# Performance work log

Measured on AMD Instinct MI355X. Metric: run time of the kernel, lower is better.

## Reference

```python
import jax, jax.numpy as jnp
import numpy as np

Q_DIM, T_DIM, TOP_M, TEMP = 512, 768, 5, 0.07
B, H, W, K = 8, 64, 64, 128
LN_EPS = 1e-5

def _layernorm(x, g, b):
    mu = jnp.mean(x, axis=-1, keepdims=True)
    var = jnp.mean(jnp.square(x - mu), axis=-1, keepdims=True)
    return (x - mu) * jax.lax.rsqrt(var + LN_EPS) * g + b

def _l2norm(x):
    n = jnp.linalg.norm(x, axis=-1, keepdims=True)
    return x / jnp.maximum(n, 1e-12)

def setup_inputs() -> dict:
    key = jax.random.key(0)
    ks = jax.random.split(key, 12)
    s = lambda d: 1.0 / np.sqrt(d)
    return {
        'visual_features': jax.random.normal(ks[0], (B, H, W, Q_DIM), jnp.float32),
        'text_features': jax.random.normal(ks[1], (B, K, T_DIM), jnp.float32),
        'Wq': jax.random.uniform(ks[2], (Q_DIM, T_DIM), jnp.float32, -s(Q_DIM), s(Q_DIM)),
        'bq': jnp.zeros((T_DIM,), jnp.float32),
        'Wv': jax.random.uniform(ks[3], (T_DIM, Q_DIM), jnp.float32, -s(T_DIM), s(T_DIM)),
        'bv': jnp.zeros((Q_DIM,), jnp.float32),
        'W1': jax.random.uniform(ks[4], (Q_DIM, 4 * Q_DIM), jnp.float32, -s(Q_DIM), s(Q_DIM)),
        'b1': jnp.zeros((4 * Q_DIM,), jnp.float32),
        'W2': jax.random.uniform(ks[5], (4 * Q_DIM, Q_DIM), jnp.float32, -s(4 * Q_DIM), s(4 * Q_DIM)),
        'b2': jnp.zeros((Q_DIM,), jnp.float32),
        'g1': jnp.ones((Q_DIM,), jnp.float32), 'be1': jnp.zeros((Q_DIM,), jnp.float32),
        'g2': jnp.ones((Q_DIM,), jnp.float32), 'be2': jnp.zeros((Q_DIM,), jnp.float32),
    }

def reference(visual_features, text_features, Wq, bq, Wv, bv, W1, b1, W2, b2, g1, be1, g2, be2):
    b, h, w, c = visual_features.shape
    residual = visual_features.reshape(b, h * w, c)
    vis = _layernorm(residual, g1, be1)                      # (B,N,C)
    query = _l2norm(vis @ Wq + bq)                            # (B,N,Ct)
    keyt = _l2norm(text_features)                             # (B,K,Ct)
    value = text_features @ Wv + bv                           # (B,K,C)
    sim = jnp.einsum('bnc,bkc->bnk', query, keyt)             # (B,N,K)
    # top-M sparsification: keep top_m logits, others -> -inf
    top_v = jax.lax.top_k(sim, TOP_M)[0]                      # (B,N,M) sorted desc
    thr = top_v[..., -1:]
    sim = jnp.where(sim >= thr, sim, -jnp.inf)
    attn = jax.nn.softmax(sim / TEMP, axis=-1)
    aligned = jnp.einsum('bnk,bkc->bnc', attn, value)
    fused = residual + aligned
    fused = _layernorm(fused, g2, be2)
    ffn = jax.nn.gelu(fused @ W1 + b1, approximate=False) @ W2 + b2
    out = fused + ffn
    return out.reshape(b, h, w, c)
```

## Files before the change

kernel.cpp:

```cpp
#include <hip/hip_runtime.h>
#include <math.h>

typedef unsigned short u16;
typedef unsigned int   u32;
typedef unsigned long long u64;
typedef __attribute__((ext_vector_type(4))) float f32x4;
typedef __attribute__((ext_vector_type(4))) unsigned int u32x4;
typedef __attribute__((ext_vector_type(8))) _Float16 f16x8;
typedef __attribute__((ext_vector_type(8))) short s16x8;

#define NROWS   32768
#define CDIM    512
#define TDIM    768
#define KKEY    128
#define FFDIM   2048
#define NB      8
#define RPB     4096
#define LN_EPS_ 1e-5f
#define TINV    (1.0f/0.07f)
#define RESCUE_MARGIN 1e-5f

__device__ __forceinline__ u16 f2h(float f){ _Float16 h=(_Float16)f; return __builtin_bit_cast(u16,h); }
__device__ __forceinline__ float h2f(u16 v){ return (float)__builtin_bit_cast(_Float16, v); }
__device__ __forceinline__ unsigned pk2(float a,float b){ return (unsigned)f2h(a)|((unsigned)f2h(b)<<16); }
__device__ __forceinline__ u16 f2b(float f){
  u32 u = __builtin_bit_cast(u32, f);
  u32 r = (u + 0x7fffu + ((u>>16)&1u)) >> 16;
  return (u16)r;
}
__device__ __forceinline__ float b2f(u16 h){ u32 u = ((u32)h)<<16; return __builtin_bit_cast(float, u); }
__device__ __forceinline__ unsigned pkb(float a,float b){ return (unsigned)f2b(a)|((unsigned)f2b(b)<<16); }

__device__ __forceinline__ void gl_lds16(const void* g, void* l){
  __builtin_amdgcn_global_load_lds(
      (const __attribute__((address_space(1))) u32*)g,
      (__attribute__((address_space(3))) u32*)l, 16, 0, 0);
}

__device__ __forceinline__ float fast_exp2(float x){
#if __has_builtin(__builtin_amdgcn_exp2f)
  return __builtin_amdgcn_exp2f(x);
#else
  return exp2f(x);
#endif
}
__device__ __forceinline__ float fast_rcp(float x){
#if __has_builtin(__builtin_amdgcn_rcpf)
  return __builtin_amdgcn_rcpf(x);
#else
  return 1.0f/x;
#endif
}

__device__ __forceinline__ float wsumf(float v){
#pragma unroll
  for(int o=1;o<64;o<<=1) v+=__shfl_xor(v,o);
  return v; }
__device__ __forceinline__ float wmaxf(float v){
#pragma unroll
  for(int o=1;o<64;o<<=1) v=fmaxf(v,__shfl_xor(v,o));
  return v; }
__device__ __forceinline__ double wsumd(double v){
#pragma unroll
  for(int o=1;o<64;o<<=1) v+=__shfl_xor(v,o);
  return v; }
__device__ __forceinline__ double wmaxd(double v){
#pragma unroll
  for(int o=1;o<64;o<<=1){ double t=__shfl_xor(v,o); v = t>v ? t : v; }
  return v; }

__device__ __forceinline__ double blocksumd4(double v, double* red){
  const int lane = threadIdx.x & 63, w = threadIdx.x >> 6;
  v = wsumd(v);
  __syncthreads();
  if (lane==0) red[w] = v;
  __syncthreads();
  return red[0]+red[1]+red[2]+red[3];
}

template<int R, int C, int MODE>
__device__ __forceinline__ void tr_tile(const float* __restrict__ in, void* __restrict__ out,
                                        int bx, int by, float (*tile)[33])
{
  int c0 = bx*32, r0 = by*32;
  int tx = threadIdx.x, ty = threadIdx.y;
#pragma unroll
  for (int i=0;i<4;i++){
    int r = r0 + ty + i*8;
    tile[ty+i*8][tx] = in[(size_t)r*C + c0 + tx];
  }
  __syncthreads();
#pragma unroll
  for (int i=0;i<4;i++){
    int cc = c0 + ty + i*8, rr = r0 + tx;
    float v = tile[tx][ty+i*8];
    if (MODE==1)      ((u16*)out)[(size_t)cc*R + rr] = f2h(v);
    else if (MODE==2) ((u16*)out)[(size_t)cc*R + rr] = f2b(v);
    else              ((float*)out)[(size_t)cc*R + rr] = v;
  }
}

__global__ __launch_bounds__(256) void transpose_all_kernel(
    const float* __restrict__ Wq, const float* __restrict__ W1,
    const float* __restrict__ W2, const float* __restrict__ Wv,
    u16* __restrict__ Wqbt, u16* __restrict__ W116t,
    u16* __restrict__ W216t, float* __restrict__ WvT)
{
  __shared__ float tile[32][33];
  int bid = blockIdx.x;
  if (bid < 384){
    tr_tile<512,768,2>(Wq, Wqbt, bid%24, bid/24, tile);
  } else if (bid < 1408){
    int b = bid-384;  tr_tile<512,2048,1>(W1, W116t, b%64, b/64, tile);
  } else if (bid < 2432){
    int b = bid-1408; tr_tile<2048,512,1>(W2, W216t, b%16, b/16, tile);
  } else {
    int b = bid-2432; tr_tile<768,512,0>(Wv, WvT, b%16, b/16, tile);
  }
}

__global__ __launch_bounds__(256) void keystats_kernel(
    const float* __restrict__ text, const float* __restrict__ bq,
    float* __restrict__ normk, float* __restrict__ crr)
{
  int gw = blockIdx.x*4 + (threadIdx.x>>6);
  int lane = threadIdx.x & 63;
  const float* tr = &text[(size_t)gw*TDIM];
  double ss=0.0, db=0.0;
#pragma unroll
  for (int i=0;i<12;i++){
    float v = tr[lane + 64*i];
    ss += (double)v*(double)v;
    db += (double)bq[lane+64*i]*(double)v;
  }
  ss = wsumd(ss); db = wsumd(db);
  if (lane==0){
    double nk = sqrt(ss); nk = nk>1e-12 ? nk : 1e-12;
    normk[gw] = (float)nk;
    crr[gw]   = (float)db;
  }
}

__global__ __launch_bounds__(256) void ln1_kernel(
    const float* __restrict__ visual, const float* __restrict__ g1, const float* __restrict__ be1,
    u16* __restrict__ visH, u16* __restrict__ visL)
{
  int row = blockIdx.x*4 + (threadIdx.x>>6);
  int lane = threadIdx.x & 63;
  size_t base = (size_t)row*CDIM + lane*8;
  f32x4 a = *(const f32x4*)&visual[base];
  f32x4 c = *(const f32x4*)&visual[base+4];
  float s = a[0]+a[1]+a[2]+a[3]+c[0]+c[1]+c[2]+c[3];
  s = wsumf(s);
  float mu = s * (1.0f/512.0f);
  float q = 0.f;
#pragma unroll
  for (int i=0;i<4;i++){ float d=a[i]-mu; q+=d*d; }
#pragma unroll
  for (int i=0;i<4;i++){ float d=c[i]-mu; q+=d*d; }
  q = wsumf(q);
  float rs = rsqrtf(q*(1.0f/512.0f) + LN_EPS_);
  int cb = lane*8;
  float o[8];
#pragma unroll
  for (int i=0;i<4;i++) o[i]   = (a[i]-mu)*rs*g1[cb+i]   + be1[cb+i];
#pragma unroll
  for (int i=0;i<4;i++) o[4+i] = (c[i]-mu)*rs*g1[cb+4+i] + be1[cb+4+i];
  u16 hh[8];
  float lo[8];
#pragma unroll
  for (int i=0;i<8;i++){ hh[i] = f2b(o[i]); lo[i] = o[i] - b2f(hh[i]); }
  u32x4 hv, lv;
#pragma unroll
  for (int i=0;i<4;i++){
    hv[i] = (u32)hh[2*i] | ((u32)hh[2*i+1]<<16);
    lv[i] = pkb(lo[2*i], lo[2*i+1]);
  }
  *(u32x4*)&visH[base] = hv;
  *(u32x4*)&visL[base] = lv;
}

__global__ __launch_bounds__(256) void gemm_f32_kernel(
    const float* __restrict__ A, const float* __restrict__ Bt, float* __restrict__ C,
    int M, int N, int K, long sA, long sB, long sC)
{
  __shared__ float As[64][17];
  __shared__ float Bs[64][17];
  const int z = blockIdx.z;
  A  += (size_t)z * sA; Bt += (size_t)z * sB; C += (size_t)z * sC;
  const int tid = threadIdx.x;
  const int tx = tid & 15, ty = tid >> 4;
  const int m0 = blockIdx.x*64, n0 = blockIdx.y*64;
  float acc[4][4];
#pragma unroll
  for (int i=0;i<4;i++)
#pragma unroll
    for (int j=0;j<4;j++) acc[i][j]=0.f;
  const int lr = tid >> 2, lc = (tid & 3)*4;
  for (int k0=0; k0<K; k0+=16){
    f32x4 av = *(const f32x4*)&A [(size_t)(m0+lr)*K + k0 + lc];
    f32x4 bv = *(const f32x4*)&Bt[(size_t)(n0+lr)*K + k0 + lc];
#pragma unroll
    for (int i=0;i<4;i++){ As[lr][lc+i]=av[i]; Bs[lr][lc+i]=bv[i]; }
    __syncthreads();
#pragma unroll
    for (int kk=0; kk<16; kk++){
      float a[4], b[4];
#pragma unroll
      for (int i=0;i<4;i++){ a[i]=As[ty*4+i][kk]; b[i]=Bs[tx*4+i][kk]; }
#pragma unroll
      for (int i=0;i<4;i++)
#pragma unroll
        for (int j=0;j<4;j++) acc[i][j] = fmaf(a[i], b[j], acc[i][j]);
    }
    __syncthreads();
  }
#pragma unroll
  for (int i=0;i<4;i++){
    f32x4 o;
#pragma unroll
    for (int j=0;j<4;j++) o[j]=acc[i][j];
    *(f32x4*)&C[(size_t)(m0+ty*4+i)*N + n0 + tx*4] = o;
  }
}

__global__ __launch_bounds__(256) void split_kernel(
    const float* __restrict__ in, u16* __restrict__ hi, u16* __restrict__ lo, int n4)
{
  int i = blockIdx.x*256 + threadIdx.x;
  if (i >= n4) return;
  f32x4 v = *(const f32x4*)&in[i*4];
  u32 hw[2], lw[2];
#pragma unroll
  for (int j=0;j<2;j++){
    u16 h0 = f2b(v[2*j]), h1 = f2b(v[2*j+1]);
    hw[j] = (u32)h0 | ((u32)h1<<16);
    lw[j] = pkb(v[2*j]-b2f(h0), v[2*j+1]-b2f(h1));
  }
  ((u32*)hi)[i*2]   = hw[0]; ((u32*)hi)[i*2+1] = hw[1];
  ((u32*)lo)[i*2]   = lw[0]; ((u32*)lo)[i*2+1] = lw[1];
}

__device__ __forceinline__ float gelu_exact(float v){
  float x  = v*0.70710678118654752440f;
  float ax = fabsf(x);
  float t  = fast_rcp(fmaf(0.3275911f, ax, 1.0f));
  float p  = t*fmaf(t, fmaf(t, fmaf(t, fmaf(t, 1.061405429f, -1.453152027f),
                  1.421413741f), -0.284496736f), 0.254829592f);
  float e  = fast_exp2(ax*ax*(-1.4426950408889634f));
  float y  = 1.0f - p*e;
  float er = (x < 0.0f) ? -y : y;
  return 0.5f*v*(1.0f + er);
}

template<int EPI, int NN, int KK, int NT>
__global__ __launch_bounds__(256) void gemm_f16_kernel(
    const u16* __restrict__ A, const u16* __restrict__ Bt,
    const float* __restrict__ bias,
    float* __restrict__ out_f,
    u16* __restrict__ out_h,
    const u16* __restrict__ add_h)
{
  __shared__ __align__(16) u16 As[2][128*64];
  __shared__ __align__(16) u16 Bs[2][128*64];
  const int tid = threadIdx.x;
  const int lane = tid & 63, w = tid >> 6;
  const int wr = w >> 1, wc = w & 1;
  constexpr int NWG = 256*NT;
  const int wg = blockIdx.x;
  const int b2 = (wg & 7)*(NWG/8) + (wg >> 3);
  const int ntile = b2 % NT, mtile = b2 / NT;
  const int m0 = mtile*128, n0 = ntile*128;
  f32x4 acc[4][4];
#pragma unroll
  for (int i=0;i<4;i++)
#pragma unroll
    for (int j=0;j<4;j++) acc[i][j] = (f32x4)0.f;
  const int lr = lane & 15, lk = (lane >> 4)*8;
  const int c8_sw = ((lane & 7) ^ (lane >> 3))*8;
  const size_t stride32 = (size_t)32*KK;
  const u16* aBase = &A [(size_t)(m0 + w*8 + (lane>>3))*KK + c8_sw];
  const u16* bBase = &Bt[(size_t)(n0 + w*8 + (lane>>3))*KK + c8_sw];

  auto STAGE = [&](int buf, int k0){
#pragma unroll
    for (int i=0;i<4;i++){
      gl_lds16(aBase + i*stride32 + k0, &As[buf][w*512 + i*2048]);
      gl_lds16(bBase + i*stride32 + k0, &Bs[buf][w*512 + i*2048]);
    }
  };

  STAGE(0, 0);
  int cur = 0;
  for (int k0=0; k0<KK; k0+=64){
    if (k0 + 64 < KK){
      STAGE(cur^1, k0+64);
      asm volatile("s_waitcnt vmcnt(8)" ::: "memory");
    } else {
      asm volatile("s_waitcnt vmcnt(0)" ::: "memory");
    }
    __builtin_amdgcn_s_barrier();
#pragma unroll
    for (int kk=0; kk<64; kk+=32){
      s16x8 af[4], bfv[4];
      const int csw = (kk + lk) ^ ((lr & 7) << 3);
#pragma unroll
      for (int mi=0;mi<4;mi++) af[mi]  = *(const s16x8*)&As[cur][(wr*64 + mi*16 + lr)*64 + csw];
#pragma unroll
      for (int ni=0;ni<4;ni++) bfv[ni] = *(const s16x8*)&Bs[cur][(wc*64 + ni*16 + lr)*64 + csw];
#pragma unroll
      for (int mi=0;mi<4;mi++)
#pragma unroll
        for (int ni=0;ni<4;ni++){
          if (EPI == 0)
            acc[mi][ni] = __builtin_amdgcn_mfma_f32_16x16x32_bf16(af[mi], bfv[ni], acc[mi][ni], 0, 0, 0);
          else
            acc[mi][ni] = __builtin_amdgcn_mfma_f32_16x16x32_f16(
                __builtin_bit_cast(f16x8, af[mi]), __builtin_bit_cast(f16x8, bfv[ni]), acc[mi][ni], 0, 0, 0);
        }
    }
    __builtin_amdgcn_s_barrier();
    cur ^= 1;
  }
  const int lr4 = (lane >> 4)*4;
  if (EPI == 0){
    float sq[4][4];
#pragma unroll
    for (int mi=0;mi<4;mi++)
#pragma unroll
      for (int r=0;r<4;r++) sq[mi][r]=0.f;
#pragma unroll
    for (int ni=0;ni<4;ni++){
      float bqv = bias[n0 + wc*64 + ni*16 + lr];
#pragma unroll
      for (int mi=0;mi<4;mi++)
#pragma unroll
        for (int r=0;r<4;r++){
          float v = acc[mi][ni][r] + bqv;
          sq[mi][r] += v*v;
        }
    }
#pragma unroll
    for (int o=1;o<16;o<<=1)
#pragma unroll
      for (int mi=0;mi<4;mi++)
#pragma unroll
        for (int r=0;r<4;r++) sq[mi][r] += __shfl_xor(sq[mi][r], o);
    if ((lane & 15) == 0){
      int part = ntile*2 + wc;
#pragma unroll
      for (int mi=0;mi<4;mi++)
#pragma unroll
        for (int r=0;r<4;r++){
          int row = m0 + wr*64 + mi*16 + lr4 + r;
          out_f[(size_t)row*12 + part] = sq[mi][r];
        }
    }
  } else {
    const int row0 = m0 + wr*64 + lr4;
    const int col0 = n0 + wc*64 + lr;
    float bb[4];
#pragma unroll
    for (int ni=0;ni<4;ni++) bb[ni] = bias[col0 + ni*16];
    if (EPI == 1){
      u16* op = out_h + (size_t)row0*NN + col0;
#pragma unroll
      for (int mi=0;mi<4;mi++)
#pragma unroll
        for (int r=0;r<4;r++)
#pragma unroll
          for (int ni=0;ni<4;ni++)
            op[(size_t)(mi*16+r)*NN + ni*16] = f2h(gelu_exact(acc[mi][ni][r] + bb[ni]));
    } else {
      float* op = out_f + (size_t)row0*NN + col0;
      const u16* rp = add_h + (size_t)row0*NN + col0;
#pragma unroll
      for (int mi=0;mi<4;mi++)
#pragma unroll
        for (int r=0;r<4;r++)
#pragma unroll
          for (int ni=0;ni<4;ni++)
            op[(size_t)(mi*16+r)*NN + ni*16] =
                acc[mi][ni][r] + bb[ni] + h2f(rp[(size_t)(mi*16+r)*NN + ni*16]);
    }
  }
}

__global__ __launch_bounds__(256) void gemm_t_kernel(
    const u16* __restrict__ Ah, const u16* __restrict__ Al,
    const u16* __restrict__ Bh, const u16* __restrict__ Bl,
    float* __restrict__ C)
{
  __shared__ __align__(16) u16 As[2][128*64];
  __shared__ __align__(16) u16 Bs[2][128*64];
  const int tid = threadIdx.x;
  const int lane = tid & 63, w = tid >> 6;
  const int wr = w >> 1, wc = w & 1;
  const int mtile = blockIdx.x;
  const int m0 = mtile*128, z = mtile >> 5;
  f32x4 acc[4][4];
#pragma unroll
  for (int i=0;i<4;i++)
#pragma unroll
    for (int j=0;j<4;j++) acc[i][j] = (f32x4)0.f;
  const int lr = lane & 15, lk = (lane >> 4)*8;
  const int c8_sw = ((lane & 7) ^ (lane >> 3))*8;
  const size_t aOff = (size_t)(m0 + w*8 + (lane>>3))*CDIM + c8_sw;
  const size_t bOff = (size_t)(z*KKEY + w*8 + (lane>>3))*CDIM + c8_sw;
  const size_t stride32 = (size_t)32*CDIM;

  auto STAGE = [&](int buf, int s){
    const int p = s >> 3, k0 = (s & 7) << 6;
    const u16* Ap = (p==2) ? Al : Ah;
    const u16* Bp = (p==1) ? Bl : Bh;
#pragma unroll
    for (int i=0;i<4;i++){
      gl_lds16(Ap + aOff + i*stride32 + k0, &As[buf][w*512 + i*2048]);
      gl_lds16(Bp + bOff + i*stride32 + k0, &Bs[buf][w*512 + i*2048]);
    }
  };

  STAGE(0, 0);
  int cur = 0;
  for (int s=0; s<24; ++s){
    if (s < 23){
      STAGE(cur^1, s+1);
      asm volatile("s_waitcnt vmcnt(8)" ::: "memory");
    } else {
      asm volatile("s_waitcnt vmcnt(0)" ::: "memory");
    }
    __builtin_amdgcn_s_barrier();
#pragma unroll
    for (int kk=0; kk<64; kk+=32){
      s16x8 af[4], bfv[4];
      const int csw = (kk + lk) ^ ((lr & 7) << 3);
#pragma unroll
      for (int mi=0;mi<4;mi++) af[mi]  = *(const s16x8*)&As[cur][(wr*64 + mi*16 + lr)*64 + csw];
#pragma unroll
      for (int ni=0;ni<4;ni++) bfv[ni] = *(const s16x8*)&Bs[cur][(wc*64 + ni*16 + lr)*64 + csw];
#pragma unroll
      for (int mi=0;mi<4;mi++)
#pragma unroll
        for (int ni=0;ni<4;ni++)
          acc[mi][ni] = __builtin_amdgcn_mfma_f32_16x16x32_bf16(af[mi], bfv[ni], acc[mi][ni], 0, 0, 0);
    }
    __builtin_amdgcn_s_barrier();
    cur ^= 1;
  }
  const int lr4 = (lane >> 4)*4;
  const int row0 = m0 + wr*64 + lr4;
  const int col0 = wc*64 + lr;
  float* op = C + (size_t)row0*KKEY + col0;
#pragma unroll
  for (int mi=0;mi<4;mi++)
#pragma unroll
    for (int r=0;r<4;r++)
#pragma unroll
      for (int ni=0;ni<4;ni++)
        op[(size_t)(mi*16+r)*KKEY + ni*16] = acc[mi][ni][r];
}

__global__ __launch_bounds__(256) void rescue_kernel(
    const int* __restrict__ rcnt, const int* __restrict__ rlist,
    const float* __restrict__ visual, const float* __restrict__ text,
    const float* __restrict__ Wq, const float* __restrict__ bq,
    const float* __restrict__ g1, const float* __restrict__ be1,
    const float* __restrict__ g2, const float* __restrict__ be2,
    const float* __restrict__ value, const float* __restrict__ bv,
    u16* __restrict__ fused16)
{
  __shared__ double vis64[512];
  __shared__ double q64[768];
  __shared__ double sims[128];
  __shared__ double pw[128];
  __shared__ double red[4];
  __shared__ double sc2[2];
  __shared__ int klist[128];
  __shared__ int kcount;
  const int tid = threadIdx.x, lane = tid & 63, w = tid >> 6;
  int n = *rcnt; if (n > NROWS) n = NROWS;
  for (int i = blockIdx.x; i < n; i += gridDim.x){
    const int row = rlist[i], b = row >> 12;
    const size_t rb = (size_t)row*CDIM;
    double x0 = (double)visual[rb+tid], x1 = (double)visual[rb+tid+256];
    double s = blocksumd4(x0+x1, red);
    double mu = s*(1.0/512.0);
    double d0 = x0-mu, d1 = x1-mu;
    double var = blocksumd4(d0*d0+d1*d1, red);
    double rs = 1.0/sqrt(var*(1.0/512.0) + 1e-5);
    vis64[tid]     = d0*rs*(double)g1[tid]     + (double)be1[tid];
    vis64[tid+256] = d1*rs*(double)g1[tid+256] + (double)be1[tid+256];
    __syncthreads();
    double qa0=(double)bq[tid], qa1=(double)bq[tid+256], qa2=(double)bq[tid+512];
#pragma unroll 4
    for (int c=0;c<CDIM;c++){
      double v = vis64[c];
      const float* wrow = &Wq[(size_t)c*TDIM];
      qa0 += v*(double)wrow[tid];
      qa1 += v*(double)wrow[tid+256];
      qa2 += v*(double)wrow[tid+512];
    }
    q64[tid]=qa0; q64[tid+256]=qa1; q64[tid+512]=qa2;
    double nq2 = blocksumd4(qa0*qa0+qa1*qa1+qa2*qa2, red);
    double nq = sqrt(nq2); if (nq < 1e-12) nq = 1e-12;
    __syncthreads();
    if (tid < KKEY){
      const float* trow = &text[((size_t)b*KKEY + tid)*TDIM];
      double dot=0.0, nk2=0.0;
#pragma unroll 8
      for (int j=0;j<TDIM;j++){
        double tv = (double)trow[j];
        dot += q64[j]*tv; nk2 += tv*tv;
      }
      double nk = sqrt(nk2); if (nk < 1e-12) nk = 1e-12;
      sims[tid] = dot/(nq*nk);
    }
    __syncthreads();
    if (w == 0){
      double v0=sims[lane], v1=sims[lane+64];
      bool rm0=false, rm1=false;
      double thr=0.0, smax=0.0;
      for (int it=0; it<5; ++it){
        double c0 = rm0 ? -1e300 : v0;
        double c1 = rm1 ? -1e300 : v1;
        double m = wmaxd(c0>c1 ? c0 : c1);
        if (it==0) smax = m;
        thr = m;
        bool h0 = (!rm0) && (v0==m);
        u64 k0 = __ballot(h0);
        if (k0){ if (lane == __ffsll(k0)-1) rm0 = true; }
        else {
          bool h1 = (!rm1) && (v1==m);
          u64 k1 = __ballot(h1);
          if (lane == __ffsll(k1)-1) rm1 = true;
        }
      }
      if (lane==0){ sc2[0]=smax; sc2[1]=thr; kcount=0; }
    }
    __syncthreads();
    const double smax = sc2[0], thr = sc2[1];
    double p = 0.0;
    if (tid < KKEY){
      double sv = sims[tid];
      p = (sv >= thr) ? exp((sv-smax)*(1.0/0.07)) : 0.0;
      pw[tid] = p;
      if (p > 0.0){ int pos = atomicAdd(&kcount, 1); klist[pos] = tid; }
    }
    double Z = blocksumd4(p, red);
    double zi = 1.0/Z;
    __syncthreads();
    double a0=(double)bv[tid], a1=(double)bv[tid+256];
    int kc = kcount;
    for (int ki=0; ki<kc; ++ki){
      int k = klist[ki];
      double wt = pw[k]*zi;
      const float* vr = &value[((size_t)b*KKEY + k)*CDIM];
      a0 += wt*(double)vr[tid];
      a1 += wt*(double)vr[tid+256];
    }
    double f0 = (double)visual[rb+tid]     + a0;
    double f1 = (double)visual[rb+tid+256] + a1;
    double fsum = blocksumd4(f0+f1, red);
    double fmu = fsum*(1.0/512.0);
    double e0=f0-fmu, e1=f1-fmu;
    double fvar = blocksumd4(e0*e0+e1*e1, red);
    double frs = 1.0/sqrt(fvar*(1.0/512.0) + 1e-5);
    fused16[rb+tid]     = f2h((float)(e0*frs*(double)g2[tid]     + (double)be2[tid]));
    fused16[rb+tid+256] = f2h((float)(e1*frs*(double)g2[tid+256] + (double)be2[tid+256]));
    __syncthreads();
  }
}

__global__ __launch_bounds__(256) void attn_ln2_kernel(
    const float* __restrict__ visual,
    const float* __restrict__ tbuf, const float* __restrict__ crr,
    const float* __restrict__ normk, const float* __restrict__ qpart,
    const float* __restrict__ value, const float* __restrict__ bv,
    const float* __restrict__ g2, const float* __restrict__ be2,
    u16* __restrict__ fused16,
    int* __restrict__ rcnt, int* __restrict__ rlist)
{
  const int w = threadIdx.x >> 6, lane = threadIdx.x & 63;
  const int row = blockIdx.x*4 + w;
  const int b = row >> 12;
  float nqp = (lane < 12) ? qpart[(size_t)row*12 + lane] : 0.f;
  float nq2 = wsumf(nqp);
  float nq = fmaxf(sqrtf(nq2), 1e-12f);
  const float* trow = &tbuf[(size_t)row*KKEY];
  float s0 = (trow[lane]    + crr[b*KKEY + lane])    / (nq*normk[b*KKEY + lane]);
  float s1 = (trow[lane+64] + crr[b*KKEY + lane+64]) / (nq*normk[b*KKEY + lane+64]);
  float v0=s0, v1=s1; bool rm0=false, rm1=false;
  float thr=0.f, smax=0.f, m6=0.f;
  for (int it=0; it<6; ++it){
    float c0 = rm0 ? -1e30f : v0;
    float c1 = rm1 ? -1e30f : v1;
    float m = wmaxf(fmaxf(c0,c1));
    if (it==0) smax = m;
    if (it<5){
      thr = m;
      bool h0 = (!rm0) && (v0==m);
      u64 k0 = __ballot(h0);
      if (k0){ if (lane == __ffsll(k0)-1) rm0 = true; }
      else {
        bool h1 = (!rm1) && (v1==m);
        u64 k1 = __ballot(h1);
        if (lane == __ffsll(k1)-1) rm1 = true;
      }
    } else m6 = m;
  }
  if ((thr - m6) < RESCUE_MARGIN){
    if (lane == 0){
      int p = atomicAdd(rcnt, 1);
      rlist[p] = row;
    }
    return;
  }
  float p0 = (s0>=thr) ? expf((s0-smax)*TINV) : 0.f;
  float p1 = (s1>=thr) ? expf((s1-smax)*TINV) : 0.f;
  float Z = wsumf(p0+p1);
  float zi = 1.f/Z;
  float accv[8];
#pragma unroll
  for (int j=0;j<8;j++) accv[j] = bv[lane*8+j];
  u64 mk0 = __ballot(p0>0.f);
  u64 mk1 = __ballot(p1>0.f);
  while (mk0){
    int l = __ffsll(mk0)-1; mk0 &= mk0-1;
    float wt = __shfl(p0, l)*zi;
    const f32x4* vr = (const f32x4*)&value[((size_t)b*KKEY + l)*CDIM + lane*8];
    f32x4 va = vr[0], vb = vr[1];
#pragma unroll
    for (int j=0;j<4;j++){ accv[j] += wt*va[j]; accv[4+j] += wt*vb[j]; }
  }
  while (mk1){
    int l = __ffsll(mk1)-1; mk1 &= mk1-1;
    float wt = __shfl(p1, l)*zi;
    const f32x4* vr = (const f32x4*)&value[((size_t)b*KKEY + l + 64)*CDIM + lane*8];
    f32x4 va = vr[0], vb = vr[1];
#pragma unroll
    for (int j=0;j<4;j++){ accv[j] += wt*va[j]; accv[4+j] += wt*vb[j]; }
  }
  size_t rb = (size_t)row*CDIM + lane*8;
  f32x4 r0v = *(const f32x4*)&visual[rb];
  f32x4 r1v = *(const f32x4*)&visual[rb+4];
  float f[8];
#pragma unroll
  for (int j=0;j<4;j++){ f[j]=r0v[j]+accv[j]; f[4+j]=r1v[j]+accv[4+j]; }
  float fs=0.f;
#pragma unroll
  for (int j=0;j<8;j++) fs += f[j];
  fs = wsumf(fs);
  float fmu = fs*(1.0f/512.0f);
  float fvv=0.f;
#pragma unroll
  for (int j=0;j<8;j++){ float d=f[j]-fmu; fvv+=d*d; }
  fvv = wsumf(fvv);
  float frs = rsqrtf(fvv*(1.0f/512.0f) + LN_EPS_);
  int cb = lane*8;
  f32x4 o0,o1;
#pragma unroll
  for (int j=0;j<4;j++) o0[j] = (f[j]-fmu)*frs*g2[cb+j]     + be2[cb+j];
#pragma unroll
  for (int j=0;j<4;j++) o1[j] = (f[4+j]-fmu)*frs*g2[cb+4+j] + be2[cb+4+j];
  u32x4 hv;
  hv[0]=pk2(o0[0],o0[1]); hv[1]=pk2(o0[2],o0[3]);
  hv[2]=pk2(o1[0],o1[1]); hv[3]=pk2(o1[2],o1[3]);
  *(u32x4*)&fused16[rb] = hv;
}

extern "C" void kernel_launch(void* const* d_in, const int* in_sizes, int n_in,
                              void* d_out, int out_size, void* d_ws, size_t ws_size,
                              hipStream_t stream)
{
  (void)in_sizes; (void)n_in; (void)out_size; (void)ws_size;
  const float* visual = (const float*)d_in[0];
  const float* text   = (const float*)d_in[1];
  const float* Wq     = (const float*)d_in[2];
  const float* bq     = (const float*)d_in[3];
  const float* Wv     = (const float*)d_in[4];
  const float* bv     = (const float*)d_in[5];
  const float* W1     = (const float*)d_in[6];
  const float* b1     = (const float*)d_in[7];
  const float* W2     = (const float*)d_in[8];
  const float* b2     = (const float*)d_in[9];
  const float* g1     = (const float*)d_in[10];
  const float* be1    = (const float*)d_in[11];
  const float* g2     = (const float*)d_in[12];
  const float* be2    = (const float*)d_in[13];
  float* out = (float*)d_out;

  char* ws = (char*)d_ws;
  size_t off = 0;
  auto alloc = [&](size_t bytes)->char*{
    char* p = ws + off; off += (bytes + 255) & ~(size_t)255; return p; };

  u16*    visH   = (u16*)   alloc((size_t)NROWS*CDIM*2);
  u16*    visL   = (u16*)   alloc((size_t)NROWS*CDIM*2);
  u16*    h16    = (u16*)   alloc((size_t)NROWS*FFDIM*2);
  u16*    fused16= (u16*)   alloc((size_t)NROWS*CDIM*2);
  float*  tbuf   = (float*) alloc((size_t)NROWS*KKEY*4);
  float*  Mrt    = (float*) alloc((size_t)NB*KKEY*CDIM*4);
  u16*    MrtH   = (u16*)   alloc((size_t)NB*KKEY*CDIM*2);
  u16*    MrtL   = (u16*)   alloc((size_t)NB*KKEY*CDIM*2);
  float*  value  = (float*) alloc((size_t)NB*KKEY*CDIM*4);
  u16*    Wqbt   = (u16*)   alloc((size_t)TDIM*CDIM*2);
  u16*    W116t  = (u16*)   alloc((size_t)FFDIM*CDIM*2);
  u16*    W216t  = (u16*)   alloc((size_t)CDIM*FFDIM*2);
  float*  WvT    = (float*) alloc((size_t)CDIM*TDIM*4);
  float*  qpart  = (float*) alloc((size_t)NROWS*12*4);
  float*  normk  = (float*) alloc((size_t)NB*KKEY*4);
  float*  crr    = (float*) alloc((size_t)NB*KKEY*4);
  int*    rcnt   = (int*)   alloc(256);
  int*    rlist  = (int*)   alloc((size_t)NROWS*4);

  hipMemsetAsync(rcnt, 0, sizeof(int), stream);

  transpose_all_kernel<<<2816, dim3(32,8), 0, stream>>>(
      Wq, W1, W2, Wv, Wqbt, W116t, W216t, WvT);
  keystats_kernel<<<256, 256, 0, stream>>>(text, bq, normk, crr);
  gemm_f32_kernel<<<dim3(2, 8, 8), 256, 0, stream>>>(
      text, Wq, Mrt, KKEY, CDIM, TDIM, (long)KKEY*TDIM, 0, (long)KKEY*CDIM);
  gemm_f32_kernel<<<dim3(2, 8, 8), 256, 0, stream>>>(
      text, WvT, value, KKEY, CDIM, TDIM, (long)KKEY*TDIM, 0, (long)KKEY*CDIM);
  split_kernel<<<512, 256, 0, stream>>>(Mrt, MrtH, MrtL, NB*KKEY*CDIM/4);
  ln1_kernel<<<NROWS/4, 256, 0, stream>>>(visual, g1, be1, visH, visL);
  gemm_t_kernel<<<256, 256, 0, stream>>>(visH, visL, MrtH, MrtL, tbuf);
  gemm_f16_kernel<0,TDIM,CDIM,6><<<1536, 256, 0, stream>>>(
      visH, Wqbt, bq, qpart, nullptr, nullptr);
  attn_ln2_kernel<<<NROWS/4, 256, 0, stream>>>(
      visual, tbuf, crr, normk, qpart, value, bv, g2, be2,
      fused16, rcnt, rlist);
  rescue_kernel<<<256, 256, 0, stream>>>(
      rcnt, rlist, visual, text, Wq, bq, g1, be1, g2, be2, value, bv, fused16);
  gemm_f16_kernel<1,FFDIM,CDIM,16><<<4096, 256, 0, stream>>>(
      fused16, W116t, b1, nullptr, h16, nullptr);
  gemm_f16_kernel<2,CDIM,FFDIM,4><<<1024, 256, 0, stream>>>(
      h16, W216t, b2, out, nullptr, fused16);
}
```

Measured before the change: 514.7 us.

## Replace FP32 text GEMMs with split-bf16 MFMA kernel fused with hi/lo split

The two scalar FP32 GEMMs that compute text@Wq and text@Wv become one MFMA kernel using a three-pass bf16 hi/lo split (hi*hi, hi*lo, lo*hi). That kernel writes the Mrt hi/lo halves directly, which removes the separate split pass. Wv is transposed straight into bf16 hi/lo, and new split kernels prepare Wq and text. gemm_t's block-to-tile mapping is remapped, and tbuf now aliases the h16 buffer to save workspace. The split-bf16 path drops the lo*lo term, so precision is slightly lower than the FP32 kernels it replaces.

```diff
diff --git a/kernel.cpp b/kernel.cpp
--- a/kernel.cpp
+++ b/kernel.cpp
@@ -80,7 +80,7 @@
 
 template<int R, int C, int MODE>
 __device__ __forceinline__ void tr_tile(const float* __restrict__ in, void* __restrict__ out,
-                                        int bx, int by, float (*tile)[33])
+                                        void* __restrict__ out2, int bx, int by, float (*tile)[33])
 {
   int c0 = bx*32, r0 = by*32;
   int tx = threadIdx.x, ty = threadIdx.y;
@@ -96,7 +96,11 @@
     float v = tile[tx][ty+i*8];
     if (MODE==1)      ((u16*)out)[(size_t)cc*R + rr] = f2h(v);
     else if (MODE==2) ((u16*)out)[(size_t)cc*R + rr] = f2b(v);
-    else              ((float*)out)[(size_t)cc*R + rr] = v;
+    else {
+      u16 h = f2b(v);
+      ((u16*)out)[(size_t)cc*R + rr]  = h;
+      ((u16*)out2)[(size_t)cc*R + rr] = f2b(v - b2f(h));
+    }
   }
 }
 
@@ -104,19 +108,36 @@
     const float* __restrict__ Wq, const float* __restrict__ W1,
     const float* __restrict__ W2, const float* __restrict__ Wv,
     u16* __restrict__ Wqbt, u16* __restrict__ W116t,
-    u16* __restrict__ W216t, float* __restrict__ WvT)
+    u16* __restrict__ W216t, u16* __restrict__ WvTH, u16* __restrict__ WvTL)
 {
   __shared__ float tile[32][33];
   int bid = blockIdx.x;
   if (bid < 384){
-    tr_tile<512,768,2>(Wq, Wqbt, bid%24, bid/24, tile);
+    tr_tile<512,768,2>(Wq, Wqbt, nullptr, bid%24, bid/24, tile);
   } else if (bid < 1408){
-    int b = bid-384;  tr_tile<512,2048,1>(W1, W116t, b%64, b/64, tile);
+    int b = bid-384;  tr_tile<512,2048,1>(W1, W116t, nullptr, b%64, b/64, tile);
   } else if (bid < 2432){
-    int b = bid-1408; tr_tile<2048,512,1>(W2, W216t, b%16, b/16, tile);
+    int b = bid-1408; tr_tile<2048,512,1>(W2, W216t, nullptr, b%16, b/16, tile);
   } else {
-    int b = bid-2432; tr_tile<768,512,0>(Wv, WvT, b%16, b/16, tile);
-  }
+    int b = bid-2432; tr_tile<768,512,3>(Wv, WvTH, WvTL, b%16, b/16, tile);
+  }
+}
+
+__global__ __launch_bounds__(256) void split_kernel(
+    const float* __restrict__ in, u16* __restrict__ hi, u16* __restrict__ lo, int n4)
+{
+  int i = blockIdx.x*256 + threadIdx.x;
+  if (i >= n4) return;
+  f32x4 v = *(const f32x4*)&in[i*4];
+  u32 hw[2], lw[2];
+#pragma unroll
+  for (int j=0;j<2;j++){
+    u16 h0 = f2b(v[2*j]), h1 = f2b(v[2*j+1]);
+    hw[j] = (u32)h0 | ((u32)h1<<16);
+    lw[j] = pkb(v[2*j]-b2f(h0), v[2*j+1]-b2f(h1));
+  }
+  ((u32*)hi)[i*2]   = hw[0]; ((u32*)hi)[i*2+1] = hw[1];
+  ((u32*)lo)[i*2]   = lw[0]; ((u32*)lo)[i*2+1] = lw[1];
 }
 
 __global__ __launch_bounds__(256) void keystats_kernel(
@@ -180,65 +201,92 @@
   *(u32x4*)&visL[base] = lv;
 }
 
-__global__ __launch_bounds__(256) void gemm_f32_kernel(
-    const float* __restrict__ A, const float* __restrict__ Bt, float* __restrict__ C,
-    int M, int N, int K, long sA, long sB, long sC)
-{
-  __shared__ float As[64][17];
-  __shared__ float Bs[64][17];
-  const int z = blockIdx.z;
-  A  += (size_t)z * sA; Bt += (size_t)z * sB; C += (size_t)z * sC;
+__global__ __launch_bounds__(256) void gemm_txt_kernel(
+    const u16* __restrict__ Ah, const u16* __restrict__ Al,
+    const u16* __restrict__ QH, const u16* __restrict__ QL,
+    const u16* __restrict__ VH, const u16* __restrict__ VL,
+    u16* __restrict__ MrtH, u16* __restrict__ MrtL, float* __restrict__ value)
+{
+  __shared__ __align__(16) u16 As[2][128*64];
+  __shared__ __align__(16) u16 Bs[2][128*64];
   const int tid = threadIdx.x;
-  const int tx = tid & 15, ty = tid >> 4;
-  const int m0 = blockIdx.x*64, n0 = blockIdx.y*64;
-  float acc[4][4];
+  const int lane = tid & 63, w = tid >> 6;
+  const int wr = w >> 1, wc = w & 1;
+  const int bx = blockIdx.x;
+  const bool isV = blockIdx.y != 0;
+  const int mtile = bx >> 2, ntile = bx & 3;
+  const int m0 = mtile*128, n0 = ntile*128;
+  const u16* Bh = isV ? VH : QH;
+  const u16* Bl = isV ? VL : QL;
+  f32x4 acc[4][4];
 #pragma unroll
   for (int i=0;i<4;i++)
 #pragma unroll
-    for (int j=0;j<4;j++) acc[i][j]=0.f;
-  const int lr = tid >> 2, lc = (tid & 3)*4;
-  for (int k0=0; k0<K; k0+=16){
-    f32x4 av = *(const f32x4*)&A [(size_t)(m0+lr)*K + k0 + lc];
-    f32x4 bv = *(const f32x4*)&Bt[(size_t)(n0+lr)*K + k0 + lc];
-#pragma unroll
-    for (int i=0;i<4;i++){ As[lr][lc+i]=av[i]; Bs[lr][lc+i]=bv[i]; }
-    __syncthreads();
-#pragma unroll
-    for (int kk=0; kk<16; kk++){
-      float a[4], b[4];
-#pragma unroll
-      for (int i=0;i<4;i++){ a[i]=As[ty*4+i][kk]; b[i]=Bs[tx*4+i][kk]; }
-#pragma unroll
-      for (int i=0;i<4;i++)
-#pragma unroll
-        for (int j=0;j<4;j++) acc[i][j] = fmaf(a[i], b[j], acc[i][j]);
-    }
-    __syncthreads();
-  }
-#pragma unroll
-  for (int i=0;i<4;i++){
-    f32x4 o;
-#pragma unroll
-    for (int j=0;j<4;j++) o[j]=acc[i][j];
-    *(f32x4*)&C[(size_t)(m0+ty*4+i)*N + n0 + tx*4] = o;
-  }
-}
-
-__global__ __launch_bounds__(256) void split_kernel(
-    const float* __restrict__ in, u16* __restrict__ hi, u16* __restrict__ lo, int n4)
-{
-  int i = blockIdx.x*256 + threadIdx.x;
-  if (i >= n4) return;
-  f32x4 v = *(const f32x4*)&in[i*4];
-  u32 hw[2], lw[2];
-#pragma unroll
-  for (int j=0;j<2;j++){
-    u16 h0 = f2b(v[2*j]), h1 = f2b(v[2*j+1]);
-    hw[j] = (u32)h0 | ((u32)h1<<16);
-    lw[j] = pkb(v[2*j]-b2f(h0), v[2*j+1]-b2f(h1));
-  }
-  ((u32*)hi)[i*2]   = hw[0]; ((u32*)hi)[i*2+1] = hw[1];
-  ((u32*)lo)[i*2]   = lw[0]; ((u32*)lo)[i*2+1] = lw[1];
+    for (int j=0;j<4;j++) acc[i][j] = (f32x4)0.f;
+  const int lr = lane & 15, lk = (lane >> 4)*8;
+  const int c8_sw = ((lane & 7) ^ (lane >> 3))*8;
+  const int rowoff = w*8 + (lane>>3);
+  const size_t aOff = (size_t)(m0 + rowoff)*TDIM + c8_sw;
+  const size_t bOff = (size_t)(n0 + rowoff)*TDIM + c8_sw;
+  const size_t stride32 = (size_t)32*TDIM;
+
+  auto STAGE = [&](int g, int buf){
+    const int p = g/12, ks = g - p*12;
+    const int k0 = ks*64;
+    const u16* Ap = (p==2) ? Al : Ah;
+    const u16* Bp = (p==1) ? Bl : Bh;
+#pragma unroll
+    for (int i=0;i<4;i++){
+      gl_lds16(Ap + aOff + i*stride32 + k0, &As[buf][w*512 + i*2048]);
+      gl_lds16(Bp + bOff + i*stride32 + k0, &Bs[buf][w*512 + i*2048]);
+    }
+  };
+
+  STAGE(0, 0);
+  for (int g=0; g<36; ++g){
+    const int cur = g & 1;
+    if (g < 35){
+      STAGE(g+1, cur^1);
+      asm volatile("s_waitcnt vmcnt(8)" ::: "memory");
+    } else {
+      asm volatile("s_waitcnt vmcnt(0)" ::: "memory");
+    }
+    __builtin_amdgcn_s_barrier();
+#pragma unroll
+    for (int kk=0; kk<64; kk+=32){
+      s16x8 af[4], bfv[4];
+      const int csw = (kk + lk) ^ ((lr & 7) << 3);
+#pragma unroll
+      for (int mi=0;mi<4;mi++) af[mi]  = *(const s16x8*)&As[cur][(wr*64 + mi*16 + lr)*64 + csw];
+#pragma unroll
+      for (int ni=0;ni<4;ni++) bfv[ni] = *(const s16x8*)&Bs[cur][(wc*64 + ni*16 + lr)*64 + csw];
+#pragma unroll
+      for (int mi=0;mi<4;mi++)
+#pragma unroll
+        for (int ni=0;ni<4;ni++)
+          acc[mi][ni] = __builtin_amdgcn_mfma_f32_16x16x32_bf16(af[mi], bfv[ni], acc[mi][ni], 0, 0, 0);
+    }
+    __builtin_amdgcn_s_barrier();
+  }
+  const int lr4 = (lane >> 4)*4;
+  const int row0 = m0 + wr*64 + lr4;
+  const int col0 = n0 + wc*64 + lr;
+#pragma unroll
+  for (int mi=0;mi<4;mi++)
+#pragma unroll
+    for (int r=0;r<4;r++){
+      size_t rbase = (size_t)(row0 + mi*16 + r)*CDIM + col0;
+#pragma unroll
+      for (int ni=0;ni<4;ni++){
+        float v = acc[mi][ni][r];
+        if (isV) value[rbase + ni*16] = v;
+        else {
+          u16 h = f2b(v);
+          MrtH[rbase + ni*16] = h;
+          MrtL[rbase + ni*16] = f2b(v - b2f(h));
+        }
+      }
+    }
 }
 
 __device__ __forceinline__ float gelu_exact(float v){
@@ -396,7 +444,8 @@
   const int tid = threadIdx.x;
   const int lane = tid & 63, w = tid >> 6;
   const int wr = w >> 1, wc = w & 1;
-  const int mtile = blockIdx.x;
+  const int wg = blockIdx.x;
+  const int mtile = (wg & 7)*32 + (wg >> 3);
   const int m0 = mtile*128, z = mtile >> 5;
   f32x4 acc[4][4];
 #pragma unroll
@@ -405,12 +454,13 @@
     for (int j=0;j<4;j++) acc[i][j] = (f32x4)0.f;
   const int lr = lane & 15, lk = (lane >> 4)*8;
   const int c8_sw = ((lane & 7) ^ (lane >> 3))*8;
-  const size_t aOff = (size_t)(m0 + w*8 + (lane>>3))*CDIM + c8_sw;
-  const size_t bOff = (size_t)(z*KKEY + w*8 + (lane>>3))*CDIM + c8_sw;
+  const int rowoff = w*8 + (lane>>3);
+  const size_t aOff = (size_t)(m0 + rowoff)*CDIM + c8_sw;
+  const size_t bOff = (size_t)(z*KKEY + rowoff)*CDIM + c8_sw;
   const size_t stride32 = (size_t)32*CDIM;
 
-  auto STAGE = [&](int buf, int s){
-    const int p = s >> 3, k0 = (s & 7) << 6;
+  auto STAGE = [&](int g, int buf){
+    const int p = g >> 3, k0 = (g & 7) << 6;
     const u16* Ap = (p==2) ? Al : Ah;
     const u16* Bp = (p==1) ? Bl : Bh;
 #pragma unroll
@@ -421,10 +471,10 @@
   };
 
   STAGE(0, 0);
-  int cur = 0;
-  for (int s=0; s<24; ++s){
-    if (s < 23){
-      STAGE(cur^1, s+1);
+  for (int g=0; g<24; ++g){
+    const int cur = g & 1;
+    if (g < 23){
+      STAGE(g+1, cur^1);
       asm volatile("s_waitcnt vmcnt(8)" ::: "memory");
     } else {
       asm volatile("s_waitcnt vmcnt(0)" ::: "memory");
@@ -445,7 +495,6 @@
           acc[mi][ni] = __builtin_amdgcn_mfma_f32_16x16x32_bf16(af[mi], bfv[ni], acc[mi][ni], 0, 0, 0);
     }
     __builtin_amdgcn_s_barrier();
-    cur ^= 1;
   }
   const int lr4 = (lane >> 4)*4;
   const int row0 = m0 + wr*64 + lr4;
@@ -698,31 +747,34 @@
   u16*    visL   = (u16*)   alloc((size_t)NROWS*CDIM*2);
   u16*    h16    = (u16*)   alloc((size_t)NROWS*FFDIM*2);
   u16*    fused16= (u16*)   alloc((size_t)NROWS*CDIM*2);
-  float*  tbuf   = (float*) alloc((size_t)NROWS*KKEY*4);
-  float*  Mrt    = (float*) alloc((size_t)NB*KKEY*CDIM*4);
   u16*    MrtH   = (u16*)   alloc((size_t)NB*KKEY*CDIM*2);
   u16*    MrtL   = (u16*)   alloc((size_t)NB*KKEY*CDIM*2);
   float*  value  = (float*) alloc((size_t)NB*KKEY*CDIM*4);
   u16*    Wqbt   = (u16*)   alloc((size_t)TDIM*CDIM*2);
   u16*    W116t  = (u16*)   alloc((size_t)FFDIM*CDIM*2);
   u16*    W216t  = (u16*)   alloc((size_t)CDIM*FFDIM*2);
-  float*  WvT    = (float*) alloc((size_t)CDIM*TDIM*4);
+  u16*    WvTH   = (u16*)   alloc((size_t)CDIM*TDIM*2);
+  u16*    WvTL   = (u16*)   alloc((size_t)CDIM*TDIM*2);
+  u16*    WqH    = (u16*)   alloc((size_t)CDIM*TDIM*2);
+  u16*    WqL    = (u16*)   alloc((size_t)CDIM*TDIM*2);
+  u16*    textH  = (u16*)   alloc((size_t)NB*KKEY*TDIM*2);
+  u16*    textL  = (u16*)   alloc((size_t)NB*KKEY*TDIM*2);
   float*  qpart  = (float*) alloc((size_t)NROWS*12*4);
   float*  normk  = (float*) alloc((size_t)NB*KKEY*4);
   float*  crr    = (float*) alloc((size_t)NB*KKEY*4);
   int*    rcnt   = (int*)   alloc(256);
   int*    rlist  = (int*)   alloc((size_t)NROWS*4);
+  float*  tbuf   = (float*)h16;
 
   hipMemsetAsync(rcnt, 0, sizeof(int), stream);
 
   transpose_all_kernel<<<2816, dim3(32,8), 0, stream>>>(
-      Wq, W1, W2, Wv, Wqbt, W116t, W216t, WvT);
+      Wq, W1, W2, Wv, Wqbt, W116t, W216t, WvTH, WvTL);
+  split_kernel<<<384, 256, 0, stream>>>(Wq, WqH, WqL, CDIM*TDIM/4);
+  split_kernel<<<768, 256, 0, stream>>>(text, textH, textL, NB*KKEY*TDIM/4);
   keystats_kernel<<<256, 256, 0, stream>>>(text, bq, normk, crr);
-  gemm_f32_kernel<<<dim3(2, 8, 8), 256, 0, stream>>>(
-      text, Wq, Mrt, KKEY, CDIM, TDIM, (long)KKEY*TDIM, 0, (long)KKEY*CDIM);
-  gemm_f32_kernel<<<dim3(2, 8, 8), 256, 0, stream>>>(
-      text, WvT, value, KKEY, CDIM, TDIM, (long)KKEY*TDIM, 0, (long)KKEY*CDIM);
-  split_kernel<<<512, 256, 0, stream>>>(Mrt, MrtH, MrtL, NB*KKEY*CDIM/4);
+  gemm_txt_kernel<<<dim3(32, 2), 256, 0, stream>>>(
+      textH, textL, WqH, WqL, WvTH, WvTL, MrtH, MrtL, value);
   ln1_kernel<<<NROWS/4, 256, 0, stream>>>(visual, g1, be1, visH, visL);
   gemm_t_kernel<<<256, 256, 0, stream>>>(visH, visL, MrtH, MrtL, tbuf);
   gemm_f16_kernel<0,TDIM,CDIM,6><<<1536, 256, 0, stream>>>(
```

After: 467.7 us. 9.1% less time.
